# Kernel optimization log

Hardware: AMD Instinct MI355X
Metric: run time of the kernel (lower is better)

## Reference

```python
import jax, jax.numpy as jnp
import numpy as np

# BitLinear (BitNet-style) constants, reconstructed from missing helpers:
#   get_qb_range(b) -> (-2^(b-1), 2^(b-1));  Qb = 2^(b-1) = 128 for bit_range=8
#   get_beta(W)  = mean(|W|)   (||W||_1 / (n*m))
#   get_gamma(W) = max(|W|)
QB = 128.0
EP = 0.01        # ep init arg: clip margin
LN_EPS = 1e-5    # nn.LayerNorm default eps
N_IN = 4096
N_OUT = 4096


def setup_inputs() -> dict:
    key = jax.random.key(0)
    kx, kw = jax.random.split(key, 2)
    x = jax.random.normal(kx, (4, 2048, N_IN), dtype=jnp.float32)
    # weight_init(): w0 ~ N(0,1); alpha = mean(w0); binarize sign(w0 - alpha)
    w0 = jax.random.normal(kw, (N_IN, N_OUT), dtype=jnp.float32)
    alpha = jnp.mean(w0)
    beta = jnp.mean(jnp.abs(w0))          # get_beta
    gamma = jnp.max(jnp.abs(w0))          # get_gamma
    w = jnp.where(w0 - alpha > 0, 1.0, -1.0).astype(jnp.float32)
    ln_gamma = jnp.ones((N_IN,), dtype=jnp.float32)   # LayerNorm weight
    ln_beta = jnp.zeros((N_IN,), dtype=jnp.float32)   # LayerNorm bias
    return {"x": x, "w": w, "ln_gamma": ln_gamma, "ln_beta": ln_beta,
            "beta": beta, "gamma": gamma}


def reference(x, w, ln_gamma, ln_beta, beta, gamma):
    # LayerNorm over last dim
    mu = jnp.mean(x, axis=-1, keepdims=True)
    var = jnp.mean(jnp.square(x - mu), axis=-1, keepdims=True)
    xn = (x - mu) * jax.lax.rsqrt(var + LN_EPS) * ln_gamma + ln_beta
    # ABSMax quantize: scale by Qb/gamma, clip to [-Qb+ep, Qb-ep] (no int cast)
    xq = jnp.clip(xn * (QB / gamma), -QB + EP, QB - EP)
    # binary-weight matmul + dequant scale beta*gamma/Qb
    y = jnp.einsum("bsi,io->bso", xq, w) * (beta * gamma / QB)
    return y
```

## Files before the change

kernel.cpp:

```cpp
#include <hip/hip_runtime.h>

using i32x4  = __attribute__((ext_vector_type(4))) int;
using i32x16 = __attribute__((ext_vector_type(16))) int;

constexpr int K_DIM = 4096;
constexpr int N_DIM = 4096;
constexpr float QBf = 128.0f;
constexpr float EPf = 0.01f;
constexpr float LN_EPSf = 1e-5f;

#define GLOAD_LDS16(gp, lp)                                                  \
    __builtin_amdgcn_global_load_lds(                                        \
        (const __attribute__((address_space(1))) void*)(gp),                 \
        (__attribute__((address_space(3))) void*)(lp), 16, 0, 0)

#define BARRIER()                                                            \
    do { asm volatile("" ::: "memory");                                      \
         __builtin_amdgcn_s_barrier();                                       \
         asm volatile("" ::: "memory"); } while (0)

#define WAIT_LGKM(N)                                                         \
    do { asm volatile("s_waitcnt lgkmcnt(" #N ")" ::: "memory");             \
         __builtin_amdgcn_sched_barrier(0); } while (0)

#define FENCE() __builtin_amdgcn_sched_barrier(0)

__global__ __launch_bounds__(256) void prep_kernel(
    const float* __restrict__ x,
    const float* __restrict__ w,
    const float* __restrict__ ln_g,
    const float* __restrict__ ln_b,
    const float* __restrict__ gamma_p,
    char* __restrict__ xq,
    char* __restrict__ wq,
    int M)
{
    const int t = threadIdx.x;

    if ((int)blockIdx.x < M) {
        const int row = blockIdx.x;
        const float4* xr4 =
            reinterpret_cast<const float4*>(x + (size_t)row * K_DIM);

        float4 v[4];
        float sum = 0.f, sumsq = 0.f;
#pragma unroll
        for (int i = 0; i < 4; ++i) {
            v[i] = xr4[t * 4 + i];
            sum += v[i].x + v[i].y + v[i].z + v[i].w;
            sumsq += v[i].x * v[i].x + v[i].y * v[i].y
                   + v[i].z * v[i].z + v[i].w * v[i].w;
        }
#pragma unroll
        for (int off = 32; off > 0; off >>= 1) {
            sum += __shfl_down(sum, off);
            sumsq += __shfl_down(sumsq, off);
        }
        __shared__ float s_sum[4], s_sq[4];
        const int lane = t & 63, wv = t >> 6;
        if (lane == 0) { s_sum[wv] = sum; s_sq[wv] = sumsq; }
        __syncthreads();
        sum = s_sum[0] + s_sum[1] + s_sum[2] + s_sum[3];
        sumsq = s_sq[0] + s_sq[1] + s_sq[2] + s_sq[3];

        const float mu = sum * (1.0f / K_DIM);
        const float var = sumsq * (1.0f / K_DIM) - mu * mu;
        const float rstd = rsqrtf(var + LN_EPSf);
        const float qs = QBf / gamma_p[0];
        const float lo = -QBf + EPf, hi = QBf - EPf;

        alignas(16) char ob[16];
#pragma unroll
        for (int i = 0; i < 4; ++i) {
            const float4 g = reinterpret_cast<const float4*>(ln_g)[t * 4 + i];
            const float4 b = reinterpret_cast<const float4*>(ln_b)[t * 4 + i];
            const float f0 = fminf(fmaxf(((v[i].x - mu) * rstd * g.x + b.x) * qs, lo), hi);
            const float f1 = fminf(fmaxf(((v[i].y - mu) * rstd * g.y + b.y) * qs, lo), hi);
            const float f2 = fminf(fmaxf(((v[i].z - mu) * rstd * g.z + b.z) * qs, lo), hi);
            const float f3 = fminf(fmaxf(((v[i].w - mu) * rstd * g.w + b.w) * qs, lo), hi);
            int x0 = (int)rintf(f0), x1 = (int)rintf(f1);
            int x2 = (int)rintf(f2), x3 = (int)rintf(f3);
            ob[i * 4 + 0] = (char)(x0 > 127 ? 127 : x0);
            ob[i * 4 + 1] = (char)(x1 > 127 ? 127 : x1);
            ob[i * 4 + 2] = (char)(x2 > 127 ? 127 : x2);
            ob[i * 4 + 3] = (char)(x3 > 127 ? 127 : x3);
        }
        *reinterpret_cast<uint4*>(xq + (size_t)row * K_DIM + t * 16) =
            *reinterpret_cast<const uint4*>(ob);
    } else {
        __shared__ char tile[64][68];
        const int bidx = blockIdx.x - M;
        const int bk = (bidx >> 6) * 64;
        const int bn = (bidx & 63) * 64;
#pragma unroll
        for (int i = 0; i < 4; ++i) {
            const int li = i * 1024 + t * 4;
            const int r = li >> 6, c = li & 63;
            const float4 vv = *reinterpret_cast<const float4*>(
                w + (size_t)(bk + r) * N_DIM + bn + c);
            tile[r][c]     = (char)vv.x;
            tile[r][c + 1] = (char)vv.y;
            tile[r][c + 2] = (char)vv.z;
            tile[r][c + 3] = (char)vv.w;
        }
        __syncthreads();
        const int n = t >> 2, kc = t & 3;
        alignas(16) char h16[16];
#pragma unroll
        for (int j = 0; j < 16; ++j) h16[j] = tile[kc * 16 + j][n];
        *reinterpret_cast<uint4*>(wq + (size_t)(bn + n) * K_DIM + bk + kc * 16) =
            *reinterpret_cast<const uint4*>(h16);
    }
}

__global__ __launch_bounds__(512, 2) void gemm_kernel(
    const char* __restrict__ A,
    const char* __restrict__ Bt,
    float* __restrict__ C,
    const float* __restrict__ beta_p,
    const float* __restrict__ gamma_p)
{
    constexpr int NT = K_DIM / 128;
    __shared__ __align__(16) char lds[131072];

    const int t = threadIdx.x;
    const int flat = blockIdx.y * gridDim.x + blockIdx.x;
    const int xcd = flat & 7;
    const int r8 = flat >> 3;
    const int by = ((xcd >> 1) << 3) + (r8 >> 3);
    const int bx = ((xcd & 1) << 3) + (r8 & 7);
    const int bm = by * 256;
    const int bn = bx * 256;

    const int lane = t & 63;
    const int w = t >> 6;
    const int wm = w >> 2;
    const int wn = w & 3;
    const int ln31 = lane & 31;
    const int lg2 = lane >> 5;

    const char* gA = A + (size_t)bm * K_DIM;
    const char* gB = Bt + (size_t)bn * K_DIM;
    const int voff = (t & 127) * K_DIM + ((t >> 7) << 4);

    const int aoff = lg2 * 2048 + (ln31 << 4);
    const int boff = lg2 * 2048 + (((wn & 1) * 64 + ln31) << 4);

#define STAGE_OP(gbase, b, roff, kt)                                          \
    do {                                                                      \
        GLOAD_LDS16((gbase) + (size_t)(kt) * 128 + voff,                      \
                    lds + (b) * 65536 + (roff) + t * 16);                     \
        GLOAD_LDS16((gbase) + (size_t)(kt) * 128 + voff + 64,                 \
                    lds + (b) * 65536 + (roff) + 8192 + t * 16);              \
        GLOAD_LDS16((gbase) + (size_t)(128 * K_DIM) + (size_t)(kt) * 128      \
                        + voff,                                               \
                    lds + (b) * 65536 + (roff) + 16384 + t * 16);             \
        GLOAD_LDS16((gbase) + (size_t)(128 * K_DIM) + (size_t)(kt) * 128      \
                        + voff + 64,                                          \
                    lds + (b) * 65536 + (roff) + 16384 + 8192 + t * 16);      \
    } while (0)

#define STAGE_A(b, kt) STAGE_OP(gA, b, 0, kt)
#define STAGE_B(b, kt) STAGE_OP(gB, b, 32768, kt)

#define LD(p) (*reinterpret_cast<const i32x4*>(p))

#define READ_A(par, ks, mfp)                                                  \
    do {                                                                      \
        afr[par][0] = LD(ab + (ks) * 4096 + (mfp) * 1024 + aoff);             \
        afr[par][1] = LD(ab + (ks) * 4096 + (mfp) * 1024 + 512 + aoff);       \
    } while (0)

#define MFMA4(par, ks, mfp)                                                   \
    do {                                                                      \
        __builtin_amdgcn_s_setprio(1);                                        \
        _Pragma("unroll")                                                     \
        for (int m2 = 0; m2 < 2; ++m2)                                        \
            _Pragma("unroll")                                                 \
            for (int nf = 0; nf < 2; ++nf)                                    \
                acc[(mfp) * 2 + m2][nf] =                                     \
                    __builtin_amdgcn_mfma_i32_32x32x32_i8(                    \
                        afr[par][m2], bfrag[nf][ks],                          \
                        acc[(mfp) * 2 + m2][nf], 0, 0, 0);                    \
        __builtin_amdgcn_s_setprio(0);                                        \
    } while (0)

#define TILE(b, tt)                                                           \
    do {                                                                      \
        const char* ab = lds + (b) * 65536 + wm * 16384;                      \
        const char* bb = lds + (b) * 65536 + 32768 + (wn >> 1) * 16384;       \
        i32x4 bfrag[2][4];                                      \
        i32x4 afr[2][2];                                    \
        _Pragma("unroll")                                                     \
        for (int nf = 0; nf < 2; ++nf)                                        \
            _Pragma("unroll")                                                 \
            for (int ks = 0; ks < 4; ++ks)                                    \
                bfrag[nf][ks] = LD(bb + ks * 4096 + nf * 512 + boff);         \
        READ_A(0, 0, 0);                                                      \
        FENCE();                                                              \
         READ_A(1, 0, 1);                                             \
        if ((tt) + 1 < NT) STAGE_A((b) ^ 1, (tt) + 1);                        \
        WAIT_LGKM(2); MFMA4(0, 0, 0);                                         \
         READ_A(0, 1, 0); WAIT_LGKM(2); MFMA4(1, 0, 1);               \
         READ_A(1, 1, 1); WAIT_LGKM(2); MFMA4(0, 1, 0);               \
         READ_A(0, 2, 0); WAIT_LGKM(2); MFMA4(1, 1, 1);               \
        BARRIER();                                                            \
         READ_A(1, 2, 1);                                             \
        if ((tt) + 2 < NT) STAGE_B(b, (tt) + 2);                              \
        WAIT_LGKM(2); MFMA4(0, 2, 0);                                         \
         READ_A(0, 3, 0); WAIT_LGKM(2); MFMA4(1, 2, 1);               \
         READ_A(1, 3, 1); WAIT_LGKM(2); MFMA4(0, 3, 0);               \
         WAIT_LGKM(0); MFMA4(1, 3, 1);                                \
        if ((tt) + 2 < NT) asm volatile("s_waitcnt vmcnt(4)" ::: "memory");   \
        else               asm volatile("s_waitcnt vmcnt(0)" ::: "memory");   \
        BARRIER();                                                            \
    } while (0)

    i32x16 acc[4][2];
#pragma unroll
    for (int m = 0; m < 4; ++m)
#pragma unroll
        for (int n = 0; n < 2; ++n)
#pragma unroll
            for (int q = 0; q < 16; ++q)
                acc[m][n][q] = 0;

    STAGE_A(0, 0); STAGE_B(0, 0); STAGE_B(1, 1);
    asm volatile("s_waitcnt vmcnt(4)" ::: "memory");
    BARRIER();

    for (int kt = 0; kt < NT; kt += 2) {
        TILE(0, kt);
        TILE(1, kt + 1);
    }

    const float scale = beta_p[0] * gamma_p[0] * (1.0f / QBf);
    const int orow0 = bm + wm * 128 + lg2 * 4;
    const int ocol0 = bn + wn * 64 + ln31;
#pragma unroll
    for (int mf = 0; mf < 4; ++mf) {
#pragma unroll
        for (int nf = 0; nf < 2; ++nf) {
#pragma unroll
            for (int reg = 0; reg < 16; ++reg) {
                const int row = orow0 + mf * 32 + (reg & 3) + 8 * (reg >> 2);
                C[(size_t)row * N_DIM + ocol0 + nf * 32] =
                    (float)acc[mf][nf][reg] * scale;
            }
        }
    }
#undef STAGE_OP
#undef STAGE_A
#undef STAGE_B
#undef LD
#undef READ_A
#undef MFMA4
#undef TILE
}

extern "C" void kernel_launch(void* const* d_in, const int* in_sizes, int n_in,
                              void* d_out, int out_size, void* d_ws, size_t ws_size,
                              hipStream_t stream)
{
    const float* x       = (const float*)d_in[0];
    const float* w       = (const float*)d_in[1];
    const float* ln_g    = (const float*)d_in[2];
    const float* ln_b    = (const float*)d_in[3];
    const float* beta_p  = (const float*)d_in[4];
    const float* gamma_p = (const float*)d_in[5];
    float* out = (float*)d_out;

    const int M = in_sizes[0] / K_DIM;

    char* xq = (char*)d_ws;
    char* wq = (char*)d_ws + (size_t)M * K_DIM;

    prep_kernel<<<M + (K_DIM / 64) * (N_DIM / 64), 256, 0, stream>>>(
        x, w, ln_g, ln_b, gamma_p, xq, wq, M);
    gemm_kernel<<<dim3(N_DIM / 256, M / 256), 512, 0, stream>>>(
        xq, wq, out, beta_p, gamma_p);
}
```

Baseline: 214.6 us.

## Pre-swizzle weights into MFMA fragment order and load B directly to registers

The weight-prep kernel now writes the transposed int8 weights in a 32x32-fragment-major layout, so each lane's MFMA B operand is a contiguous 16-byte chunk. The GEMM loads B fragments straight from global memory into registers, one tile ahead, instead of staging them through LDS. This halves LDS usage and drops one barrier per tile. In exchange, B reads are no longer shared across waves through LDS, so each wave fetches its own B from global/L2, and more registers stay live for the prefetched fragments.

```diff
diff --git a/kernel.cpp b/kernel.cpp
--- a/kernel.cpp
+++ b/kernel.cpp
@@ -108,7 +108,13 @@
         alignas(16) char h16[16];
 #pragma unroll
         for (int j = 0; j < 16; ++j) h16[j] = tile[kc * 16 + j][n];
-        *reinterpret_cast<uint4*>(wq + (size_t)(bn + n) * K_DIM + bk + kc * 16) =
+        const int gn = bn + n;
+        const int gk = bk + kc * 16;
+        const int n32 = gn >> 5;
+        const int k32 = gk >> 5;
+        const int l   = ((gk >> 4) & 1) * 32 + (gn & 31);
+        *reinterpret_cast<uint4*>(
+            wq + ((size_t)(n32 * (K_DIM / 32) + k32) * 64 + l) * 16) =
             *reinterpret_cast<const uint4*>(h16);
     }
 }
@@ -121,7 +127,7 @@
     const float* __restrict__ gamma_p)
 {
     constexpr int NT = K_DIM / 128;
-    __shared__ __align__(16) char lds[131072];
+    __shared__ __align__(16) char lds[65536];
 
     const int t = threadIdx.x;
     const int flat = blockIdx.y * gridDim.x + blockIdx.x;
@@ -140,28 +146,27 @@
     const int lg2 = lane >> 5;
 
     const char* gA = A + (size_t)bm * K_DIM;
-    const char* gB = Bt + (size_t)bn * K_DIM;
     const int voff = (t & 127) * K_DIM + ((t >> 7) << 4);
 
     const int aoff = lg2 * 2048 + (ln31 << 4);
-    const int boff = lg2 * 2048 + (((wn & 1) * 64 + ln31) << 4);
-
-#define STAGE_OP(gbase, b, roff, kt)                                          \
-    do {                                                                      \
-        GLOAD_LDS16((gbase) + (size_t)(kt) * 128 + voff,                      \
-                    lds + (b) * 65536 + (roff) + t * 16);                     \
-        GLOAD_LDS16((gbase) + (size_t)(kt) * 128 + voff + 64,                 \
-                    lds + (b) * 65536 + (roff) + 8192 + t * 16);              \
-        GLOAD_LDS16((gbase) + (size_t)(128 * K_DIM) + (size_t)(kt) * 128      \
-                        + voff,                                               \
-                    lds + (b) * 65536 + (roff) + 16384 + t * 16);             \
-        GLOAD_LDS16((gbase) + (size_t)(128 * K_DIM) + (size_t)(kt) * 128      \
-                        + voff + 64,                                          \
-                    lds + (b) * 65536 + (roff) + 16384 + 8192 + t * 16);      \
-    } while (0)
-
-#define STAGE_A(b, kt) STAGE_OP(gA, b, 0, kt)
-#define STAGE_B(b, kt) STAGE_OP(gB, b, 32768, kt)
+
+    const char* gB0 = Bt + ((size_t)((bn >> 5) + wn * 2)     * 128) * 1024
+                         + (size_t)lane * 16;
+    const char* gB1 = Bt + ((size_t)((bn >> 5) + wn * 2 + 1) * 128) * 1024
+                         + (size_t)lane * 16;
+
+#define STAGE_A(b, kt)                                                        \
+    do {                                                                      \
+        GLOAD_LDS16(gA + (size_t)(kt) * 128 + voff,                           \
+                    lds + (b) * 32768 + t * 16);                              \
+        GLOAD_LDS16(gA + (size_t)(kt) * 128 + voff + 64,                      \
+                    lds + (b) * 32768 + 8192 + t * 16);                       \
+        GLOAD_LDS16(gA + (size_t)(128 * K_DIM) + (size_t)(kt) * 128 + voff,   \
+                    lds + (b) * 32768 + 16384 + t * 16);                      \
+        GLOAD_LDS16(gA + (size_t)(128 * K_DIM) + (size_t)(kt) * 128 + voff    \
+                        + 64,                                                 \
+                    lds + (b) * 32768 + 16384 + 8192 + t * 16);               \
+    } while (0)
 
 #define LD(p) (*reinterpret_cast<const i32x4*>(p))
 
@@ -169,6 +174,15 @@
     do {                                                                      \
         afr[par][0] = LD(ab + (ks) * 4096 + (mfp) * 1024 + aoff);             \
         afr[par][1] = LD(ab + (ks) * 4096 + (mfp) * 1024 + 512 + aoff);       \
+    } while (0)
+
+#define READ_B(kt1)                                                           \
+    do {                                                                      \
+        _Pragma("unroll")                                                     \
+        for (int ks = 0; ks < 4; ++ks) {                                      \
+            bfrag[ks][0] = LD(gB0 + (size_t)(kt1) * 4096 + ks * 1024);        \
+            bfrag[ks][1] = LD(gB1 + (size_t)(kt1) * 4096 + ks * 1024);        \
+        }                                                                     \
     } while (0)
 
 #define MFMA4(par, ks, mfp)                                                   \
@@ -180,39 +194,28 @@
             for (int nf = 0; nf < 2; ++nf)                                    \
                 acc[(mfp) * 2 + m2][nf] =                                     \
                     __builtin_amdgcn_mfma_i32_32x32x32_i8(                    \
-                        afr[par][m2], bfrag[nf][ks],                          \
+                        afr[par][m2], bfrag[ks][nf],                          \
                         acc[(mfp) * 2 + m2][nf], 0, 0, 0);                    \
         __builtin_amdgcn_s_setprio(0);                                        \
     } while (0)
 
-#define TILE(b, tt)                                                           \
-    do {                                                                      \
-        const char* ab = lds + (b) * 65536 + wm * 16384;                      \
-        const char* bb = lds + (b) * 65536 + 32768 + (wn >> 1) * 16384;       \
-        i32x4 bfrag[2][4];                                      \
-        i32x4 afr[2][2];                                    \
-        _Pragma("unroll")                                                     \
-        for (int nf = 0; nf < 2; ++nf)                                        \
-            _Pragma("unroll")                                                 \
-            for (int ks = 0; ks < 4; ++ks)                                    \
-                bfrag[nf][ks] = LD(bb + ks * 4096 + nf * 512 + boff);         \
+#define TILE(b, tt, STA, RDB, VM)                                             \
+    do {                                                                      \
+        const char* ab = lds + (b) * 32768 + wm * 16384;                      \
         READ_A(0, 0, 0);                                                      \
         FENCE();                                                              \
          READ_A(1, 0, 1);                                             \
-        if ((tt) + 1 < NT) STAGE_A((b) ^ 1, (tt) + 1);                        \
+        if (STA) STAGE_A((b) ^ 1, (tt) + 1);                                  \
         WAIT_LGKM(2); MFMA4(0, 0, 0);                                         \
          READ_A(0, 1, 0); WAIT_LGKM(2); MFMA4(1, 0, 1);               \
          READ_A(1, 1, 1); WAIT_LGKM(2); MFMA4(0, 1, 0);               \
          READ_A(0, 2, 0); WAIT_LGKM(2); MFMA4(1, 1, 1);               \
-        BARRIER();                                                            \
-         READ_A(1, 2, 1);                                             \
-        if ((tt) + 2 < NT) STAGE_B(b, (tt) + 2);                              \
-        WAIT_LGKM(2); MFMA4(0, 2, 0);                                         \
+         READ_A(1, 2, 1); WAIT_LGKM(2); MFMA4(0, 2, 0);               \
          READ_A(0, 3, 0); WAIT_LGKM(2); MFMA4(1, 2, 1);               \
          READ_A(1, 3, 1); WAIT_LGKM(2); MFMA4(0, 3, 0);               \
          WAIT_LGKM(0); MFMA4(1, 3, 1);                                \
-        if ((tt) + 2 < NT) asm volatile("s_waitcnt vmcnt(4)" ::: "memory");   \
-        else               asm volatile("s_waitcnt vmcnt(0)" ::: "memory");   \
+        if (RDB) READ_B((tt) + 1);                                            \
+        asm volatile("s_waitcnt vmcnt(" #VM ")" ::: "memory");                \
         BARRIER();                                                            \
     } while (0)
 
@@ -225,14 +228,20 @@
             for (int q = 0; q < 16; ++q)
                 acc[m][n][q] = 0;
 
-    STAGE_A(0, 0); STAGE_B(0, 0); STAGE_B(1, 1);
-    asm volatile("s_waitcnt vmcnt(4)" ::: "memory");
+    i32x4 afr[2][2];
+    i32x4 bfrag[4][2];
+
+    STAGE_A(0, 0);
+    READ_B(0);
+    asm volatile("s_waitcnt vmcnt(8)" ::: "memory");
     BARRIER();
 
-    for (int kt = 0; kt < NT; kt += 2) {
-        TILE(0, kt);
-        TILE(1, kt + 1);
+    for (int kt = 0; kt < NT - 2; kt += 2) {
+        TILE(0, kt, 1, 1, 8);
+        TILE(1, kt + 1, 1, 1, 8);
     }
+    TILE(0, NT - 2, 1, 1, 8);
+    TILE(1, NT - 1, 0, 0, 0);
 
     const float scale = beta_p[0] * gamma_p[0] * (1.0f / QBf);
     const int orow0 = bm + wm * 128 + lg2 * 4;
@@ -249,11 +258,10 @@
             }
         }
     }
-#undef STAGE_OP
 #undef STAGE_A
-#undef STAGE_B
 #undef LD
 #undef READ_A
+#undef READ_B
 #undef MFMA4
 #undef TILE
 }
```

New measurement: 217.8 us. About the same (+1.5%).
